# Kernel tuning notes

Hardware: AMD Instinct MI355X
Metric: run time of the kernel (lower is better)

The kernel has to match this reference:

```python
import jax, jax.numpy as jnp
import numpy as np

B, H, S, D = 4, 16, 2048, 64
NEG_INF = -1e9  # matches torch masked_fill value of -1000000000.0


def setup_inputs() -> dict:
    key = jax.random.key(0)
    kq, kk, kv = jax.random.split(key, 3)
    query = jax.random.normal(kq, (B, H, S, D), dtype=jnp.float32)
    key_t = jax.random.normal(kk, (B, H, S, D), dtype=jnp.float32)
    value = jax.random.normal(kv, (B, H, S, D), dtype=jnp.float32)
    # causal mask, broadcast over batch and heads; 0 = masked out
    mask = jnp.tril(jnp.ones((S, S), dtype=jnp.int32))[None, None]
    return {"query": query, "key": key_t, "value": value, "mask": mask}


def reference(query, key, value, mask):
    d = query.shape[-1]
    scale = 1.0 / jnp.sqrt(jnp.float32(d))
    # [B,H,S,S] attention scores
    attn_score = jnp.einsum("bhqd,bhkd->bhqk", query, key) * scale
    masked = jnp.where(mask == 0, NEG_INF, attn_score)
    attn_prob = jax.nn.softmax(masked, axis=-1)
    out = jnp.einsum("bhqk,bhkd->bhqd", attn_prob, value)
    return out, attn_prob
```

## Files before the change

### kernel.cpp

```cpp
#include <hip/hip_runtime.h>
#include <hip/hip_bf16.h>


#define S_DIM 2048
#define D_DIM 64
#define NBH   64
#define SC2   0.18033688011112042f

typedef __attribute__((ext_vector_type(4))) float f32x4;
typedef __attribute__((ext_vector_type(8))) short bf16x8;
typedef __attribute__((ext_vector_type(4))) short bf16x4;
typedef __attribute__((ext_vector_type(4))) float floatx4;

static __device__ __forceinline__ ushort f2bf(float x) {
    __hip_bfloat16 h = __float2bfloat16(x);
    return *reinterpret_cast<ushort*>(&h);
}
static __device__ __forceinline__ bf16x8 pack8(floatx4 a, floatx4 b) {
    bf16x8 r;
    r[0]=(short)f2bf(a[0]); r[1]=(short)f2bf(a[1]); r[2]=(short)f2bf(a[2]); r[3]=(short)f2bf(a[3]);
    r[4]=(short)f2bf(b[0]); r[5]=(short)f2bf(b[1]); r[6]=(short)f2bf(b[2]); r[7]=(short)f2bf(b[3]);
    return r;
}
static __device__ __forceinline__ bf16x4 pack4f(float a, float b, float c, float d) {
    bf16x4 r;
    r[0]=(short)f2bf(a); r[1]=(short)f2bf(b); r[2]=(short)f2bf(c); r[3]=(short)f2bf(d);
    return r;
}
#define MFMA(a, b, acc) __builtin_amdgcn_mfma_f32_16x16x32_bf16((a), (b), (acc), 0, 0, 0)
#define BARLDS() asm volatile("s_waitcnt lgkmcnt(0)\n\ts_barrier" ::: "memory")
#define NT4(p, v) __builtin_nontemporal_store((v), (floatx4*)(p))

__global__ __launch_bounds__(256, 3) void attn_fwd_kernel(
    const float* __restrict__ Q, const float* __restrict__ K,
    const float* __restrict__ V, float* __restrict__ Out,
    float* __restrict__ Attn)
{
    __shared__ __align__(16) ushort KtR[2][64][72];
    __shared__ __align__(16) ushort Vt[2][64][72];
    __shared__ __align__(16) ushort Pl[4][16][40];

    const int tid = threadIdx.x;
    const int id  = blockIdx.x;

    if (id % 3 == 2) {
        const int z  = id / 3;
        const int bh = z >> 3;
        const int j  = z & 7;
        float* Attnb = Attn + (size_t)bh * (size_t)S_DIM * S_DIM;
        const floatx4 z4 = {0.f, 0.f, 0.f, 0.f};
        const int ct0 = (z % 31);
        for (int s = 0; s < 31; ++s) {
            int ct = ct0 + s; if (ct >= 31) ct -= 31;
            ct += 1;
            const int nr = ct << 3;
            float* base = Attnb + (ct << 6) + ((tid & 15) << 2);
            for (int i = (tid >> 4); i < nr; i += 16) {
                const int r = j + (i << 3);
                NT4(base + (size_t)r * S_DIM, z4);
            }
        }
        return;
    }

    const int cid  = (id / 3) * 2 + (id % 3);
    const int w    = tid >> 6;
    const int lane = tid & 63;
    const int g    = lane >> 4;
    const int c    = lane & 15;

    const int xpr  = cid >> 6;
    const int bh   = cid & 63;

    const float* Qb = Q + (size_t)bh * S_DIM * D_DIM;
    const float* Kb = K + (size_t)bh * S_DIM * D_DIM;
    const float* Vb = V + (size_t)bh * S_DIM * D_DIM;
    float* Outb  = Out  + (size_t)bh * S_DIM * D_DIM;
    float* Attnb = Attn + (size_t)bh * (size_t)S_DIM * S_DIM;

    const int q0L = xpr << 6;
    const int q0H = (31 - xpr) << 6;
    const int qrL = q0L + (w << 4) + c;
    const int qrH = q0H + (w << 4) + c;
    const int NTL1 = xpr + 1;
    const int NT1  = 32 - xpr;
    const int phase = cid % NT1;

    float* AttnL = Attnb + (size_t)qrL * S_DIM;
    float* AttnH = Attnb + (size_t)qrH * S_DIM;

    bf16x8 bQL0, bQL1, bQH0, bQH1;
    {
        const float* qp = Qb + (size_t)qrL * D_DIM + (g << 3);
        bQL0 = pack8(*(const floatx4*)qp,        *(const floatx4*)(qp + 4));
        bQL1 = pack8(*(const floatx4*)(qp + 32), *(const floatx4*)(qp + 36));
        qp = Qb + (size_t)qrH * D_DIM + (g << 3);
        bQH0 = pack8(*(const floatx4*)qp,        *(const floatx4*)(qp + 4));
        bQH1 = pack8(*(const floatx4*)(qp + 32), *(const floatx4*)(qp + 36));
    }

    const int kr1 = tid >> 2;
    const int kc1 = (tid & 3) << 4;
    const int vd  = tid & 63;
    const int vg16 = (tid >> 6) << 4;

    floatx4 kA, kB, kC, kD;
    {
        const float* s = Kb + ((size_t)(phase << 6) + kr1) * D_DIM + kc1;
        kA = *(const floatx4*)s;      kB = *(const floatx4*)(s + 4);
        kC = *(const floatx4*)(s + 8); kD = *(const floatx4*)(s + 12);
    }
    float laccL = 0.0f, laccH = 0.0f;

    int tq = phase;
    for (int t = 0; t < NT1; ++t) {
        ushort (*kt)[72] = KtR[t & 1];
        *(bf16x8*)&kt[kr1][kc1]     = pack8(kA, kB);
        *(bf16x8*)&kt[kr1][kc1 + 8] = pack8(kC, kD);
        BARLDS();
        const int tq1 = (tq + 1 == NT1) ? 0 : tq + 1;
        if (t + 1 < NT1) {
            const float* s = Kb + ((size_t)(tq1 << 6) + kr1) * D_DIM + kc1;
            kA = *(const floatx4*)s;       kB = *(const floatx4*)(s + 4);
            kC = *(const floatx4*)(s + 8); kD = *(const floatx4*)(s + 12);
        }
        const bool doL   = (tq < NTL1);
        const bool lastL = (tq == xpr);
        const bool lastH = (tq == NT1 - 1);
        #pragma unroll
        for (int h = 0; h < 4; ++h) {
            const bf16x8 a0 = *(const bf16x8*)&kt[(h << 4) + c][(g << 3)];
            const bf16x8 a1 = *(const bf16x8*)&kt[(h << 4) + c][(g << 3) + 32];
            f32x4 AH = {0.f, 0.f, 0.f, 0.f};
            AH = MFMA(a0, bQH0, AH);
            AH = MFMA(a1, bQH1, AH);
            #pragma unroll
            for (int r = 0; r < 4; ++r) {
                float v = AH[r] * SC2;
                if (lastH && ((tq << 6) + (h << 4) + (g << 2) + r) > qrH) v = -1e30f;
                laccH += exp2f(v);
            }
            if (doL) {
                f32x4 AL = {0.f, 0.f, 0.f, 0.f};
                AL = MFMA(a0, bQL0, AL);
                AL = MFMA(a1, bQL1, AL);
                #pragma unroll
                for (int r = 0; r < 4; ++r) {
                    float v = AL[r] * SC2;
                    if (lastL && ((tq << 6) + (h << 4) + (g << 2) + r) > qrL) v = -1e30f;
                    laccL += exp2f(v);
                }
            }
        }
        tq = tq1;
    }

    float vv[16];
    {
        const float* s = Kb + ((size_t)(phase << 6) + kr1) * D_DIM + kc1;
        kA = *(const floatx4*)s;      kB = *(const floatx4*)(s + 4);
        kC = *(const floatx4*)(s + 8); kD = *(const floatx4*)(s + 12);
        const float* sv = Vb + ((size_t)(phase << 6) + vg16) * D_DIM + vd;
        #pragma unroll
        for (int i = 0; i < 16; ++i) vv[i] = sv[(size_t)i * D_DIM];
    }

    laccL += __shfl_xor(laccL, 16);
    laccL += __shfl_xor(laccL, 32);
    laccH += __shfl_xor(laccH, 16);
    laccH += __shfl_xor(laccH, 32);
    const float linvL = 1.0f / laccL;
    const float linvH = 1.0f / laccH;

    BARLDS();

    f32x4 oL[4], oH[4];
    #pragma unroll
    for (int nb = 0; nb < 4; ++nb) {
        oL[nb] = (f32x4){0.f, 0.f, 0.f, 0.f};
        oH[nb] = (f32x4){0.f, 0.f, 0.f, 0.f};
    }

    tq = phase;
    for (int t = 0; t < NT1; ++t) {
        const int buf = t & 1;
        ushort (*kt)[72] = KtR[buf];
        *(bf16x8*)&kt[kr1][kc1]     = pack8(kA, kB);
        *(bf16x8*)&kt[kr1][kc1 + 8] = pack8(kC, kD);
        *(bf16x4*)&Vt[buf][vd][vg16]      = pack4f(vv[0],  vv[1],  vv[2],  vv[3]);
        *(bf16x4*)&Vt[buf][vd][vg16 + 4]  = pack4f(vv[4],  vv[5],  vv[6],  vv[7]);
        *(bf16x4*)&Vt[buf][vd][vg16 + 8]  = pack4f(vv[8],  vv[9],  vv[10], vv[11]);
        *(bf16x4*)&Vt[buf][vd][vg16 + 12] = pack4f(vv[12], vv[13], vv[14], vv[15]);
        BARLDS();
        const int tq1 = (tq + 1 == NT1) ? 0 : tq + 1;
        if (t + 1 < NT1) {
            const float* s = Kb + ((size_t)(tq1 << 6) + kr1) * D_DIM + kc1;
            kA = *(const floatx4*)s;       kB = *(const floatx4*)(s + 4);
            kC = *(const floatx4*)(s + 8); kD = *(const floatx4*)(s + 12);
            const float* sv = Vb + ((size_t)(tq1 << 6) + vg16) * D_DIM + vd;
            #pragma unroll
            for (int i = 0; i < 16; ++i) vv[i] = sv[(size_t)i * D_DIM];
        }
        const bool doL = (tq < NTL1);
        const bool mL  = (tq == xpr);
        const bool mH  = (tq == NT1 - 1);

        #pragma unroll
        for (int sl = 0; sl < 2; ++sl) {
            const bf16x8 vb0 = *(const bf16x8*)&Vt[buf][c     ][(sl << 5) + (g << 3)];
            const bf16x8 vb1 = *(const bf16x8*)&Vt[buf][c + 16][(sl << 5) + (g << 3)];
            const bf16x8 vb2 = *(const bf16x8*)&Vt[buf][c + 32][(sl << 5) + (g << 3)];
            const bf16x8 vb3 = *(const bf16x8*)&Vt[buf][c + 48][(sl << 5) + (g << 3)];

            #pragma unroll
            for (int h = 0; h < 2; ++h) {
                const int row = (sl << 5) + (h << 4) + c;
                const bf16x8 a0 = *(const bf16x8*)&kt[row][(g << 3)];
                const bf16x8 a1 = *(const bf16x8*)&kt[row][(g << 3) + 32];
                f32x4 AH = {0.f, 0.f, 0.f, 0.f};
                AH = MFMA(a0, bQH0, AH);
                AH = MFMA(a1, bQH1, AH);
                floatx4 pv;
                #pragma unroll
                for (int r = 0; r < 4; ++r) {
                    float v = AH[r] * SC2;
                    if (mH && ((tq << 6) + (sl << 5) + (h << 4) + (g << 2) + r) > qrH) v = -1e30f;
                    pv[r] = exp2f(v) * linvH;
                }
                NT4(AttnH + (tq << 6) + (sl << 5) + (h << 4) + (g << 2), pv);
                *(bf16x4*)&Pl[w][c][(h << 4) + (g << 2)] = pack4f(pv[0], pv[1], pv[2], pv[3]);
            }
            {
                const bf16x8 pa = *(const bf16x8*)&Pl[w][c][g << 3];
                oH[0] = MFMA(pa, vb0, oH[0]);
                oH[1] = MFMA(pa, vb1, oH[1]);
                oH[2] = MFMA(pa, vb2, oH[2]);
                oH[3] = MFMA(pa, vb3, oH[3]);
            }

            if (doL) {
                #pragma unroll
                for (int h = 0; h < 2; ++h) {
                    const int row = (sl << 5) + (h << 4) + c;
                    const bf16x8 a0 = *(const bf16x8*)&kt[row][(g << 3)];
                    const bf16x8 a1 = *(const bf16x8*)&kt[row][(g << 3) + 32];
                    f32x4 AL = {0.f, 0.f, 0.f, 0.f};
                    AL = MFMA(a0, bQL0, AL);
                    AL = MFMA(a1, bQL1, AL);
                    floatx4 pl;
                    #pragma unroll
                    for (int r = 0; r < 4; ++r) {
                        float v = AL[r] * SC2;
                        if (mL && ((tq << 6) + (sl << 5) + (h << 4) + (g << 2) + r) > qrL) v = -1e30f;
                        pl[r] = exp2f(v) * linvL;
                    }
                    NT4(AttnL + (tq << 6) + (sl << 5) + (h << 4) + (g << 2), pl);
                    *(bf16x4*)&Pl[w][c][(h << 4) + (g << 2)] = pack4f(pl[0], pl[1], pl[2], pl[3]);
                }
                const bf16x8 pa = *(const bf16x8*)&Pl[w][c][g << 3];
                oL[0] = MFMA(pa, vb0, oL[0]);
                oL[1] = MFMA(pa, vb1, oL[1]);
                oL[2] = MFMA(pa, vb2, oL[2]);
                oL[3] = MFMA(pa, vb3, oL[3]);
            }
        }
        tq = tq1;
    }

    #pragma unroll
    for (int r = 0; r < 4; ++r) {
        float* op = Outb + (size_t)(q0L + (w << 4) + (g << 2) + r) * D_DIM + c;
        __builtin_nontemporal_store(oL[0][r], op);
        __builtin_nontemporal_store(oL[1][r], op + 16);
        __builtin_nontemporal_store(oL[2][r], op + 32);
        __builtin_nontemporal_store(oL[3][r], op + 48);
        op = Outb + (size_t)(q0H + (w << 4) + (g << 2) + r) * D_DIM + c;
        __builtin_nontemporal_store(oH[0][r], op);
        __builtin_nontemporal_store(oH[1][r], op + 16);
        __builtin_nontemporal_store(oH[2][r], op + 32);
        __builtin_nontemporal_store(oH[3][r], op + 48);
    }
}

extern "C" void kernel_launch(void* const* d_in, const int* in_sizes, int n_in,
                              void* d_out, int out_size, void* d_ws, size_t ws_size,
                              hipStream_t stream) {
    const float* Q = (const float*)d_in[0];
    const float* K = (const float*)d_in[1];
    const float* V = (const float*)d_in[2];
    float* out  = (float*)d_out;
    float* attn = out + (size_t)NBH * S_DIM * D_DIM;

    attn_fwd_kernel<<<dim3(1536), 256, 0, stream>>>(Q, K, V, out, attn);
}
```

Before: 323.4 us.

## Fold zero-fill of masked attention into a fifth wave per compute block

The separate zero-fill blocks that wrote the masked upper triangle of the attention matrix are replaced by an extra wavefront in each compute block. That wave spreads its zero stores across the block's barrier count, so the fill is interleaved with the compute waves' MFMA work. The grid shrinks from 1536 to 1024 blocks of 320 threads, and the launch-bounds occupancy hint is dropped. This risks register pressure and occupancy changes, and the barrier counting must exactly match the compute path's barrier count or the block will deadlock.

Result: faster. 301.0 us (-6.9%).

```diff
diff --git a/kernel.cpp b/kernel.cpp
--- a/kernel.cpp
+++ b/kernel.cpp
@@ -31,7 +31,7 @@
 #define BARLDS() asm volatile("s_waitcnt lgkmcnt(0)\n\ts_barrier" ::: "memory")
 #define NT4(p, v) __builtin_nontemporal_store((v), (floatx4*)(p))
 
-__global__ __launch_bounds__(256, 3) void attn_fwd_kernel(
+__global__ __launch_bounds__(320) void attn_fwd_kernel(
     const float* __restrict__ Q, const float* __restrict__ K,
     const float* __restrict__ V, float* __restrict__ Out,
     float* __restrict__ Attn)
@@ -43,48 +43,48 @@
     const int tid = threadIdx.x;
     const int id  = blockIdx.x;
 
-    if (id % 3 == 2) {
-        const int z  = id / 3;
-        const int bh = z >> 3;
-        const int j  = z & 7;
-        float* Attnb = Attn + (size_t)bh * (size_t)S_DIM * S_DIM;
-        const floatx4 z4 = {0.f, 0.f, 0.f, 0.f};
-        const int ct0 = (z % 31);
-        for (int s = 0; s < 31; ++s) {
-            int ct = ct0 + s; if (ct >= 31) ct -= 31;
-            ct += 1;
-            const int nr = ct << 3;
-            float* base = Attnb + (ct << 6) + ((tid & 15) << 2);
-            for (int i = (tid >> 4); i < nr; i += 16) {
-                const int r = j + (i << 3);
+    const int xpr = id >> 6;
+    const int bh  = id & 63;
+    const int NT1  = 32 - xpr;
+    const int NTL1 = xpr + 1;
+
+    float* Attnb = Attn + (size_t)bh * (size_t)S_DIM * S_DIM;
+    const floatx4 z4 = {0.f, 0.f, 0.f, 0.f};
+
+    if (tid >= 256) {
+        const int lane = tid & 63;
+        const int lr   = lane >> 4;
+        const int lc   = (lane & 15) << 2;
+        int bars = 2 * NT1 + 1;
+        const int per = (496 + bars - 1) / bars;
+        int cnt = 0;
+        for (int ct = 1; ct <= 31; ++ct) {
+            float* base = Attnb + (ct << 6) + lc;
+            for (int j = 0; j < ct; ++j) {
+                const int r = xpr + ((lr + (j << 2)) << 4);
                 NT4(base + (size_t)r * S_DIM, z4);
-            }
-        }
+                if (++cnt == per) { BARLDS(); --bars; cnt = 0; }
+            }
+        }
+        while (bars-- > 0) BARLDS();
         return;
     }
 
-    const int cid  = (id / 3) * 2 + (id % 3);
     const int w    = tid >> 6;
     const int lane = tid & 63;
     const int g    = lane >> 4;
     const int c    = lane & 15;
 
-    const int xpr  = cid >> 6;
-    const int bh   = cid & 63;
-
     const float* Qb = Q + (size_t)bh * S_DIM * D_DIM;
     const float* Kb = K + (size_t)bh * S_DIM * D_DIM;
     const float* Vb = V + (size_t)bh * S_DIM * D_DIM;
-    float* Outb  = Out  + (size_t)bh * S_DIM * D_DIM;
-    float* Attnb = Attn + (size_t)bh * (size_t)S_DIM * S_DIM;
+    float* Outb = Out + (size_t)bh * S_DIM * D_DIM;
 
     const int q0L = xpr << 6;
     const int q0H = (31 - xpr) << 6;
     const int qrL = q0L + (w << 4) + c;
     const int qrH = q0H + (w << 4) + c;
-    const int NTL1 = xpr + 1;
-    const int NT1  = 32 - xpr;
-    const int phase = cid % NT1;
+    const int phase = id % NT1;
 
     float* AttnL = Attnb + (size_t)qrL * S_DIM;
     float* AttnH = Attnb + (size_t)qrH * S_DIM;
@@ -291,5 +291,5 @@
     float* out  = (float*)d_out;
     float* attn = out + (size_t)NBH * S_DIM * D_DIM;
 
-    attn_fwd_kernel<<<dim3(1536), 256, 0, stream>>>(Q, K, V, out, attn);
-}
+    attn_fwd_kernel<<<dim3(1024), 320, 0, stream>>>(Q, K, V, out, attn);
+}
```
